# Performance work log

Hardware: AMD Instinct MI355X
Metric: run time of the kernel (lower is better)

## Reference

```python
import jax, jax.numpy as jnp
import numpy as np
import math

KERNEL_SIZES = [3, 5, 7, 7, 9, 9]
DILATIONS = [1, 2, 1, 3, 1, 2]
NUM_HEADS = 6
HEAD_DIM = 32  # in_channels 192 / 6 heads


def _neighborhood_patches(t, k, dil):
    """Equivalent of F.unfold(t, kernel_size=k, dilation=dil, padding=dil*(k//2)).
    t: [B, d, H, W] -> [B, d, k*k, H, W] (zero-padded borders, torch unfold ordering:
    patch index p = i*k + j over the kernel window, row-major)."""
    B, d, H, W = t.shape
    pad = dil * (k // 2)
    tp = jnp.pad(t, ((0, 0), (0, 0), (pad, pad), (pad, pad)))
    pats = [tp[:, :, i * dil:i * dil + H, j * dil:j * dil + W]
            for i in range(k) for j in range(k)]
    return jnp.stack(pats, axis=2)


def setup_inputs() -> dict:
    key = jax.random.key(0)
    ks = jax.random.split(key, 3 + NUM_HEADS)
    B, C, H, W = 4, 192, 96, 96
    x = jax.random.normal(ks[0], (B, C, H, W), dtype=jnp.float32)
    w_qkv = jax.random.normal(ks[1], (3 * C, C), dtype=jnp.float32) * 0.02  # 1x1 conv weight
    w_out = jax.random.normal(ks[2], (C, C), dtype=jnp.float32) * 0.02      # 1x1 conv weight
    inp = {"x": x, "w_qkv": w_qkv, "w_out": w_out}
    for i, k in enumerate(KERNEL_SIZES):
        # module inits biases to zeros; use small randn so softmax path is exercised
        inp[f"b{i}"] = jax.random.normal(ks[3 + i], (k * k,), dtype=jnp.float32) * 0.02
    return inp


def reference(x, w_qkv, w_out, b0, b1, b2, b3, b4, b5):
    biases = [b0, b1, b2, b3, b4, b5]
    B, C, H, W = x.shape
    scale = 1.0 / math.sqrt(HEAD_DIM)
    # 1x1 conv qkv projection
    qkv = jnp.einsum('bchw,oc->bohw', x, w_qkv)
    q, k, v = jnp.split(qkv, 3, axis=1)
    q = q.reshape(B, NUM_HEADS, HEAD_DIM, H, W)
    k = k.reshape(B, NUM_HEADS, HEAD_DIM, H, W)
    v = v.reshape(B, NUM_HEADS, HEAD_DIM, H, W)
    head_outs = []
    for i in range(NUM_HEADS):  # heads have structurally different (k, dilation)
        ksz, dil = KERNEL_SIZES[i], DILATIONS[i]
        kp = _neighborhood_patches(k[:, i], ksz, dil)  # [B, d, k*k, H, W]
        vp = _neighborhood_patches(v[:, i], ksz, dil)  # [B, d, k*k, H, W]
        scores = jnp.einsum('bdhw,bdphw->bphw', q[:, i], kp) * scale
        scores = scores + biases[i][None, :, None, None]
        attn = jax.nn.softmax(scores, axis=1)  # softmax over the k*k neighborhood
        head_outs.append(jnp.einsum('bphw,bdphw->bdhw', attn, vp))
    out = jnp.concatenate(head_outs, axis=1)  # [B, C, H, W]
    return jnp.einsum('bchw,oc->bohw', out, w_out)
```

## Files before the change

kernel.cpp:

```cpp
#include <hip/hip_runtime.h>
#include <hip/hip_bf16.h>
#include <math.h>

#define NPIX 9216
#define HDIM 96
#define WDIM 96
#define NHEADS 6
#define BATCH 4

typedef _Float16 f16x8 __attribute__((ext_vector_type(8)));
typedef float    f32x4 __attribute__((ext_vector_type(4)));

struct Bias6 { const float* p[6]; };

__device__ __forceinline__ void cp16(void* ldst, const void* gsrc) {
    __builtin_amdgcn_global_load_lds(
        (const __attribute__((address_space(1))) unsigned int*)gsrc,
        (__attribute__((address_space(3))) unsigned int*)ldst, 16, 0, 0);
}

__device__ __forceinline__ unsigned packf16(float a, float b) {
    _Float16 ha = (_Float16)a, hb = (_Float16)b;
    return (unsigned)*(unsigned short*)&ha | ((unsigned)*(unsigned short*)&hb << 16);
}

template<int N>
__device__ __forceinline__ void waitcnt_vm() {
    if constexpr (N == 0) asm volatile("s_waitcnt vmcnt(0)" ::: "memory");
    else if constexpr (N == 2) asm volatile("s_waitcnt vmcnt(2)" ::: "memory");
    else if constexpr (N == 3) asm volatile("s_waitcnt vmcnt(3)" ::: "memory");
    else if constexpr (N == 4) asm volatile("s_waitcnt vmcnt(4)" ::: "memory");
    else asm volatile("s_waitcnt vmcnt(0)" ::: "memory");
    __builtin_amdgcn_sched_barrier(0);
}

#define MIX_LL(acc, kk, qq) asm("v_fma_mix_f32 %0, %1, %2, %0 op_sel:[0,0,0] op_sel_hi:[1,1,0]" : "+v"(acc) : "v"(kk), "v"(qq))
#define MIX_HH(acc, kk, qq) asm("v_fma_mix_f32 %0, %1, %2, %0 op_sel:[1,1,0] op_sel_hi:[1,1,0]" : "+v"(acc) : "v"(kk), "v"(qq))
#define MIX_LF(acc, vv, ee) asm("v_fma_mix_f32 %0, %1, %2, %0 op_sel:[0,0,0] op_sel_hi:[1,0,0]" : "+v"(acc) : "v"(vv), "v"(ee))
#define MIX_HF(acc, vv, ee) asm("v_fma_mix_f32 %0, %1, %2, %0 op_sel:[1,0,0] op_sel_hi:[1,0,0]" : "+v"(acc) : "v"(vv), "v"(ee))

__global__ __launch_bounds__(256) void convert_x(
    const float* __restrict__ x, _Float16* __restrict__ Xf,
    const float* __restrict__ w1, _Float16* __restrict__ Wf1,
    const float* __restrict__ w2, _Float16* __restrict__ Wf2,
    uint4* __restrict__ guard)
{
    __shared__ float t[32][65];
    const int b  = blockIdx.z;
    const int c0 = blockIdx.y * 32;
    const int p0 = blockIdx.x * 64;
    const int tid = threadIdx.x;

    if (blockIdx.y == 0 && blockIdx.z == 0) {
        const int f = blockIdx.x * 256 + tid;
        #pragma unroll
        for (int u = 0; u < 4; ++u) {
            const int i = f * 4 + u;
            if (i < 576 * 192) Wf1[i] = (_Float16)w1[i];
            else               Wf2[i - 576 * 192] = (_Float16)w2[i - 576 * 192];
        }
        if (blockIdx.x == 0 && tid < 64)
            guard[tid] = make_uint4(0u, 0u, 0u, 0u);
    }

    const int pl = tid & 63;
    #pragma unroll
    for (int i = 0; i < 8; ++i) {
        const int c = i * 4 + (tid >> 6);
        t[c][pl] = x[((size_t)b * 192 + c0 + c) * NPIX + p0 + pl];
    }
    __syncthreads();
    const int p  = tid >> 2;
    const int cq = (tid & 3) * 8;
    f16x8 vh;
    #pragma unroll
    for (int j = 0; j < 8; ++j)
        vh[j] = (_Float16)t[cq + j][p];
    *(f16x8*)(Xf + ((size_t)b * NPIX + p0 + p) * 192 + c0 + cq) = vh;
}

template<int MODE, int M>
__global__ __launch_bounds__(256) void gemm_mfma(
    const _Float16* __restrict__ A, const _Float16* __restrict__ B,
    void* __restrict__ Yv)
{
    constexpr int MT = M / 64;
    __shared__ _Float16 sA[64 * 64];
    __shared__ _Float16 sB[128 * 64];

    const int orig = blockIdx.x;
    const int xcd = orig & 7;
    const int l = orig >> 3;
    const int m0 = (l % MT) * 64;
    const int b  = (l / MT) & 3;
    const int n0 = (xcd * 9 + l / (MT * 4)) * 128;

    const int tid  = threadIdx.x;
    const int lane = tid & 63;
    const int wid  = tid >> 6;
    const int wr = wid >> 1, wc = wid & 1;
    const int lr = lane & 15;
    const int kg = lane >> 4;

    const char* gA = (const char*)A + (size_t)m0 * 384;
    const char* gB = (const char*)B + ((size_t)b * NPIX + n0) * 384;

    f32x4 acc[2][4];
    #pragma unroll
    for (int mf = 0; mf < 2; ++mf)
        #pragma unroll
        for (int nf = 0; nf < 4; ++nf)
            acc[mf][nf] = (f32x4){0.f, 0.f, 0.f, 0.f};

    for (int ks = 0; ks < 3; ++ks) {
        if (ks) __syncthreads();
        const int kb = ks * 128;
        #pragma unroll
        for (int it = 0; it < 2; ++it) {
            const int d  = it * 256 + tid;
            const int rd = d >> 3, cd = d & 7;
            const size_t src = (size_t)rd * 384 + kb + ((cd ^ (rd & 7)) << 4);
            cp16((char*)sA + d * 16, gA + src);
        }
        #pragma unroll
        for (int it = 0; it < 4; ++it) {
            const int d  = it * 256 + tid;
            const int rd = d >> 3, cd = d & 7;
            const size_t src = (size_t)rd * 384 + kb + ((cd ^ (rd & 7)) << 4);
            cp16((char*)sB + d * 16, gB + src);
        }
        __syncthreads();
        #pragma unroll
        for (int s = 0; s < 2; ++s) {
            f16x8 aH[2], bH[4];
            #pragma unroll
            for (int mf = 0; mf < 2; ++mf) {
                const int row = wr * 32 + mf * 16 + lr;
                const int c = (s * 4 + kg) ^ (row & 7);
                aH[mf] = *(const f16x8*)((const char*)sA + row * 128 + c * 16);
            }
            #pragma unroll
            for (int nf = 0; nf < 4; ++nf) {
                const int row = wc * 64 + nf * 16 + lr;
                const int c = (s * 4 + kg) ^ (row & 7);
                bH[nf] = *(const f16x8*)((const char*)sB + row * 128 + c * 16);
            }
            #pragma unroll
            for (int mf = 0; mf < 2; ++mf)
                #pragma unroll
                for (int nf = 0; nf < 4; ++nf)
                    acc[mf][nf] = __builtin_amdgcn_mfma_f32_16x16x32_f16(aH[mf], bH[nf], acc[mf][nf], 0, 0, 0);
        }
    }

    if (MODE == 0) {
        float* Yb = (float*)Yv + ((size_t)b * M + m0 + wr * 32) * NPIX + n0 + wc * 64;
        #pragma unroll
        for (int mf = 0; mf < 2; ++mf)
            #pragma unroll
            for (int r = 0; r < 4; ++r) {
                const int row = mf * 16 + kg * 4 + r;
                #pragma unroll
                for (int nf = 0; nf < 4; ++nf)
                    Yb[(size_t)row * NPIX + nf * 16 + lr] = acc[mf][nf][r];
            }
    } else {
        #pragma unroll
        for (int mf = 0; mf < 2; ++mf) {
            const int cbase = m0 + wr * 32 + mf * 16 + kg * 4;
            unsigned* Yq = (unsigned*)Yv
                + (((size_t)b * 72 + (cbase >> 3)) * NPIX + n0 + wc * 64 + lr) * 4
                + ((kg & 1) << 1);
            #pragma unroll
            for (int nf = 0; nf < 4; ++nf) {
                Yq[(nf * 16) * 4 + 0] = packf16(acc[mf][nf][0], acc[mf][nf][1]);
                Yq[(nf * 16) * 4 + 1] = packf16(acc[mf][nf][2], acc[mf][nf][3]);
            }
        }
    }
}

#define TW 16
#define TH 16

template<int KSZ, int DIL, bool DB, int L>
__device__ __forceinline__ void attn_body(
    const uint4* __restrict__ Qq, const uint4* __restrict__ Kq,
    const uint4* __restrict__ Vq, const float* __restrict__ bias,
    const uint4* __restrict__ guard,
    _Float16* __restrict__ oh, int h0, int w0,
    uint4* __restrict__ bufs,
    unsigned (* __restrict__ out_lds)[256])
{
    constexpr int CC  = KSZ / 2;
    constexpr int HAL = CC * DIL;
    constexpr int R   = TH + 2 * HAL;
    constexpr int C   = TW + 2 * HAL;
    constexpr int RC  = R * C;
    constexpr int NN  = KSZ * KSZ;

    const int tid = threadIdx.x;
    const int tx = tid & 15;
    const int ty = tid >> 4;
    const int pix = (h0 + ty) * WDIM + (w0 + tx);
    const int lb = ty * C + tx;

    uint4 qv[4];
    #pragma unroll
    for (int p = 0; p < 4; ++p) qv[p] = Qq[(size_t)p * NPIX + pix];

    float score[NN];
    #pragma unroll
    for (int n = 0; n < NN; ++n) score[n] = bias[n] * 5.656854249492381f;

    auto STAGE = [&](int r) {
        const uint4* src = (r < 4) ? (Kq + (size_t)r * NPIX)
                                   : (Vq + (size_t)(r - 4) * NPIX);
        uint4* dst = bufs + (DB ? ((r & 1) * (L * 256)) : 0);
        #pragma unroll
        for (int it = 0; it < L; ++it) {
            const int idx = it * 256 + tid;
            const int rr = idx / C, cc = idx - rr * C;
            const int gh = h0 - HAL + rr, gw = w0 - HAL + cc;
            const bool ok = (idx < RC) && ((unsigned)gh < (unsigned)HDIM)
                                       && ((unsigned)gw < (unsigned)WDIM);
            const uint4* s = ok ? (src + gh * WDIM + gw) : guard;
            cp16(dst + idx, s);
        }
    };

    auto QK = [&](const uint4* buf, int oct) {
        const uint4 q = qv[oct];
        #pragma unroll
        for (int i = 0; i < KSZ; ++i)
            #pragma unroll
            for (int j = 0; j < KSZ; ++j) {
                const uint4 k8 = buf[lb + i * DIL * C + j * DIL];
                float s = score[i * KSZ + j];
                MIX_LL(s, k8.x, q.x); MIX_HH(s, k8.x, q.x);
                MIX_LL(s, k8.y, q.y); MIX_HH(s, k8.y, q.y);
                MIX_LL(s, k8.z, q.z); MIX_HH(s, k8.z, q.z);
                MIX_LL(s, k8.w, q.w); MIX_HH(s, k8.w, q.w);
                score[i * KSZ + j] = s;
            }
    };

    float inv = 0.f;
    auto SOFTMAX = [&]() {
        float l = 0.f;
        #pragma unroll
        for (int n = 0; n < NN; ++n) {
            const float e = exp2f(score[n] * 0.25506113952980654f);
            l += e;
            score[n] = e;
        }
        inv = 1.f / l;
    };

    auto PV = [&](const uint4* buf, int oct) {
        float a0 = 0.f, a1 = 0.f, a2 = 0.f, a3 = 0.f;
        float a4 = 0.f, a5 = 0.f, a6 = 0.f, a7 = 0.f;
        #pragma unroll
        for (int i = 0; i < KSZ; ++i)
            #pragma unroll
            for (int j = 0; j < KSZ; ++j) {
                const uint4 v8 = buf[lb + i * DIL * C + j * DIL];
                const float e = score[i * KSZ + j];
                MIX_LF(a0, v8.x, e); MIX_HF(a1, v8.x, e);
                MIX_LF(a2, v8.y, e); MIX_HF(a3, v8.y, e);
                MIX_LF(a4, v8.z, e); MIX_HF(a5, v8.z, e);
                MIX_LF(a6, v8.w, e); MIX_HF(a7, v8.w, e);
            }
        const int rr = oct & 1;
        out_lds[rr * 4 + 0][tid] = packf16(a0 * inv, a1 * inv);
        out_lds[rr * 4 + 1][tid] = packf16(a2 * inv, a3 * inv);
        out_lds[rr * 4 + 2][tid] = packf16(a4 * inv, a5 * inv);
        out_lds[rr * 4 + 3][tid] = packf16(a6 * inv, a7 * inv);
    };

    auto COOP = [&](int half) {
        #pragma unroll
        for (int it = 0; it < 2; ++it) {
            const int linear = it * 256 + tid;
            const int px = linear >> 1;
            const int c  = linear & 1;
            const int gpix = (h0 + (px >> 4)) * WDIM + w0 + (px & 15);
            uint4 val = make_uint4(out_lds[c * 4 + 0][px], out_lds[c * 4 + 1][px],
                                   out_lds[c * 4 + 2][px], out_lds[c * 4 + 3][px]);
            *((uint4*)((unsigned*)(oh + (size_t)gpix * 192)) + half * 2 + c) = val;
        }
    };

    if constexpr (DB) {
        STAGE(0);
        #pragma unroll
        for (int r = 0; r < 8; ++r) {
            if (r < 7) STAGE(r + 1);
            if (r < 7) waitcnt_vm<L>(); else waitcnt_vm<0>();
            __builtin_amdgcn_s_barrier();
            __builtin_amdgcn_sched_barrier(0);
            const uint4* buf = bufs + (r & 1) * (L * 256);
            if (r < 4) {
                QK(buf, r);
                if (r == 3) SOFTMAX();
            } else {
                PV(buf, r - 4);
                asm volatile("s_waitcnt lgkmcnt(0)" ::: "memory");
                __builtin_amdgcn_sched_barrier(0);
            }
            __builtin_amdgcn_s_barrier();
            __builtin_amdgcn_sched_barrier(0);
            if (r == 5) COOP(0);
            if (r == 7) COOP(1);
        }
    } else {
        #pragma unroll
        for (int r = 0; r < 8; ++r) {
            __syncthreads();
            if (r == 6) COOP(0);
            STAGE(r);
            __syncthreads();
            const uint4* buf = bufs;
            if (r < 4) {
                QK(buf, r);
                if (r == 3) SOFTMAX();
            } else {
                PV(buf, r - 4);
            }
        }
        __syncthreads();
        COOP(1);
    }
}

__global__ __launch_bounds__(256) void attn_kernel(
    const uint4* __restrict__ qkv, Bias6 bs, _Float16* __restrict__ ATf,
    const uint4* __restrict__ guard)
{
    __shared__ uint4 bufs[1536];
    __shared__ unsigned out_lds[8][256];

    const int orig = blockIdx.x;
    const int wg = (orig & 7) * 108 + (orig >> 3);
    const int panel = wg / 36;
    const int tile = wg - panel * 36;
    const int chunk = panel / 3, slot = panel - chunk * 3;
    int head, b;
    if (slot == 0)      { head = 4 + (chunk >> 2); b = chunk & 3; }
    else if (slot == 1) { head = 2 + (chunk >> 2); b = chunk & 3; }
    else                { head = (chunk < 4) ? 1 : 0; b = chunk & 3; }
    const int txt = tile % 6, tyt = tile / 6;
    const int w0 = txt * TW, h0 = tyt * TH;

    const uint4* base = qkv + (size_t)b * 72 * NPIX;
    const uint4* Qq = base + (size_t)(head * 4) * NPIX;
    const uint4* Kq = base + (size_t)(24 + head * 4) * NPIX;
    const uint4* Vq = base + (size_t)(48 + head * 4) * NPIX;
    _Float16* oh = ATf + (size_t)b * NPIX * 192 + head * 32;
    const float* bias = bs.p[head];

    switch (head) {
        case 0: attn_body<3, 1, true, 2>(Qq, Kq, Vq, bias, guard, oh, h0, w0, bufs, out_lds); break;
        case 1: attn_body<5, 2, true, 3>(Qq, Kq, Vq, bias, guard, oh, h0, w0, bufs, out_lds); break;
        case 2: attn_body<7, 1, true, 2>(Qq, Kq, Vq, bias, guard, oh, h0, w0, bufs, out_lds); break;
        case 3: attn_body<7, 3, false, 5>(Qq, Kq, Vq, bias, guard, oh, h0, w0, bufs, out_lds); break;
        case 4: attn_body<9, 1, true, 3>(Qq, Kq, Vq, bias, guard, oh, h0, w0, bufs, out_lds); break;
        case 5: attn_body<9, 2, false, 4>(Qq, Kq, Vq, bias, guard, oh, h0, w0, bufs, out_lds); break;
    }
}

extern "C" void kernel_launch(void* const* d_in, const int* in_sizes, int n_in,
                              void* d_out, int out_size, void* d_ws, size_t ws_size,
                              hipStream_t stream) {
    const float* x     = (const float*)d_in[0];
    const float* w_qkv = (const float*)d_in[1];
    const float* w_out = (const float*)d_in[2];
    Bias6 bs;
    for (int i = 0; i < 6; ++i) bs.p[i] = (const float*)d_in[3 + i];
    float* out = (float*)d_out;

    char* ws = (char*)d_ws;
    uint4*    QKV = (uint4*)ws;         ws += (size_t)BATCH * 72 * NPIX * 16;
    _Float16* Xf  = (_Float16*)ws;      ws += (size_t)BATCH * NPIX * 192 * 2;
    _Float16* ATf = (_Float16*)ws;      ws += (size_t)BATCH * NPIX * 192 * 2;
    _Float16* Wf1 = (_Float16*)ws;      ws += (size_t)576 * 192 * 2;
    _Float16* Wf2 = (_Float16*)ws;      ws += (size_t)192 * 192 * 2;
    uint4* guard  = (uint4*)ws;         ws += 1024;

    convert_x<<<dim3(NPIX / 64, 192 / 32, BATCH), 256, 0, stream>>>(
        x, Xf, w_qkv, Wf1, w_out, Wf2, guard);

    gemm_mfma<1, 576><<<dim3(8 * (576 / 64) * 4 * 9), 256, 0, stream>>>(
        Wf1, Xf, (void*)QKV);

    attn_kernel<<<dim3(864), 256, 0, stream>>>(QKV, bs, ATf, guard);

    gemm_mfma<0, 192><<<dim3(8 * (192 / 64) * 4 * 9), 256, 0, stream>>>(
        Wf2, ATf, (void*)out);
}
```

Measured before the change: 83.27 us.

## Fuse fp32-to-fp16 conversion of inputs and weights into GEMM tile loads

Removes the separate convert_x kernel and its fp16 workspace copies of x and the weights. The GEMMs now read fp32 directly, convert to fp16 in registers and write swizzled tiles to LDS, and the guard reset moves into the first GEMM. This saves one launch and a full write and read of the converted activation tensor. In exchange, the async global-to-LDS copies for those operands become synchronous register loads, and with MT=9 each x tile is re-read and re-converted by nine M-tile blocks.

```diff
diff --git a/kernel.cpp b/kernel.cpp
--- a/kernel.cpp
+++ b/kernel.cpp
@@ -39,50 +39,10 @@
 #define MIX_LF(acc, vv, ee) asm("v_fma_mix_f32 %0, %1, %2, %0 op_sel:[0,0,0] op_sel_hi:[1,0,0]" : "+v"(acc) : "v"(vv), "v"(ee))
 #define MIX_HF(acc, vv, ee) asm("v_fma_mix_f32 %0, %1, %2, %0 op_sel:[1,0,0] op_sel_hi:[1,0,0]" : "+v"(acc) : "v"(vv), "v"(ee))
 
-__global__ __launch_bounds__(256) void convert_x(
-    const float* __restrict__ x, _Float16* __restrict__ Xf,
-    const float* __restrict__ w1, _Float16* __restrict__ Wf1,
-    const float* __restrict__ w2, _Float16* __restrict__ Wf2,
-    uint4* __restrict__ guard)
-{
-    __shared__ float t[32][65];
-    const int b  = blockIdx.z;
-    const int c0 = blockIdx.y * 32;
-    const int p0 = blockIdx.x * 64;
-    const int tid = threadIdx.x;
-
-    if (blockIdx.y == 0 && blockIdx.z == 0) {
-        const int f = blockIdx.x * 256 + tid;
-        #pragma unroll
-        for (int u = 0; u < 4; ++u) {
-            const int i = f * 4 + u;
-            if (i < 576 * 192) Wf1[i] = (_Float16)w1[i];
-            else               Wf2[i - 576 * 192] = (_Float16)w2[i - 576 * 192];
-        }
-        if (blockIdx.x == 0 && tid < 64)
-            guard[tid] = make_uint4(0u, 0u, 0u, 0u);
-    }
-
-    const int pl = tid & 63;
-    #pragma unroll
-    for (int i = 0; i < 8; ++i) {
-        const int c = i * 4 + (tid >> 6);
-        t[c][pl] = x[((size_t)b * 192 + c0 + c) * NPIX + p0 + pl];
-    }
-    __syncthreads();
-    const int p  = tid >> 2;
-    const int cq = (tid & 3) * 8;
-    f16x8 vh;
-    #pragma unroll
-    for (int j = 0; j < 8; ++j)
-        vh[j] = (_Float16)t[cq + j][p];
-    *(f16x8*)(Xf + ((size_t)b * NPIX + p0 + p) * 192 + c0 + cq) = vh;
-}
-
-template<int MODE, int M>
+template<int MODE, int M, bool BF32>
 __global__ __launch_bounds__(256) void gemm_mfma(
-    const _Float16* __restrict__ A, const _Float16* __restrict__ B,
-    void* __restrict__ Yv)
+    const float* __restrict__ A32, const void* __restrict__ Bp,
+    void* __restrict__ Yv, uint4* __restrict__ guard)
 {
     constexpr int MT = M / 64;
     __shared__ _Float16 sA[64 * 64];
@@ -102,8 +62,8 @@
     const int lr = lane & 15;
     const int kg = lane >> 4;
 
-    const char* gA = (const char*)A + (size_t)m0 * 384;
-    const char* gB = (const char*)B + ((size_t)b * NPIX + n0) * 384;
+    if (MODE == 1 && orig == 0 && tid < 64)
+        guard[tid] = make_uint4(0u, 0u, 0u, 0u);
 
     f32x4 acc[2][4];
     #pragma unroll
@@ -112,22 +72,60 @@
         for (int nf = 0; nf < 4; ++nf)
             acc[mf][nf] = (f32x4){0.f, 0.f, 0.f, 0.f};
 
+    const int ar = tid >> 2;
+    const int ac = (tid & 3) * 16;
+    const int bpx = tid & 127;
+    const int bc0 = (tid >> 7) * 32;
+
     for (int ks = 0; ks < 3; ++ks) {
         if (ks) __syncthreads();
-        const int kb = ks * 128;
-        #pragma unroll
-        for (int it = 0; it < 2; ++it) {
-            const int d  = it * 256 + tid;
-            const int rd = d >> 3, cd = d & 7;
-            const size_t src = (size_t)rd * 384 + kb + ((cd ^ (rd & 7)) << 4);
-            cp16((char*)sA + d * 16, gA + src);
-        }
-        #pragma unroll
-        for (int it = 0; it < 4; ++it) {
-            const int d  = it * 256 + tid;
-            const int rd = d >> 3, cd = d & 7;
-            const size_t src = (size_t)rd * 384 + kb + ((cd ^ (rd & 7)) << 4);
-            cp16((char*)sB + d * 16, gB + src);
+        {
+            const float* g = A32 + (size_t)(m0 + ar) * 192 + ks * 64 + ac;
+            float v[16];
+            #pragma unroll
+            for (int j = 0; j < 4; ++j) {
+                f32x4 t = *(const f32x4*)(g + j * 4);
+                v[j * 4 + 0] = t[0]; v[j * 4 + 1] = t[1];
+                v[j * 4 + 2] = t[2]; v[j * 4 + 3] = t[3];
+            }
+            #pragma unroll
+            for (int q = 0; q < 2; ++q) {
+                const int cd = (tid & 3) * 2 + q;
+                uint4 u = make_uint4(
+                    packf16(v[q * 8 + 0], v[q * 8 + 1]),
+                    packf16(v[q * 8 + 2], v[q * 8 + 3]),
+                    packf16(v[q * 8 + 4], v[q * 8 + 5]),
+                    packf16(v[q * 8 + 6], v[q * 8 + 7]));
+                *(uint4*)((char*)sA + ar * 128 + ((cd ^ (ar & 7)) << 4)) = u;
+            }
+        }
+        if constexpr (BF32) {
+            const float* g = (const float*)Bp
+                + ((size_t)b * 192 + ks * 64 + bc0) * NPIX + n0 + bpx;
+            float v[32];
+            #pragma unroll
+            for (int c = 0; c < 32; ++c)
+                v[c] = g[(size_t)c * NPIX];
+            #pragma unroll
+            for (int q = 0; q < 4; ++q) {
+                const int cd = (bc0 >> 3) + q;
+                uint4 u = make_uint4(
+                    packf16(v[q * 8 + 0], v[q * 8 + 1]),
+                    packf16(v[q * 8 + 2], v[q * 8 + 3]),
+                    packf16(v[q * 8 + 4], v[q * 8 + 5]),
+                    packf16(v[q * 8 + 6], v[q * 8 + 7]));
+                *(uint4*)((char*)sB + bpx * 128 + ((cd ^ (bpx & 7)) << 4)) = u;
+            }
+        } else {
+            const char* gB = (const char*)Bp + ((size_t)b * NPIX + n0) * 384;
+            const int kb = ks * 128;
+            #pragma unroll
+            for (int it = 0; it < 4; ++it) {
+                const int d  = it * 256 + tid;
+                const int rd = d >> 3, cd = d & 7;
+                const size_t src = (size_t)rd * 384 + kb + ((cd ^ (rd & 7)) << 4);
+                cp16((char*)sB + d * 16, gB + src);
+            }
         }
         __syncthreads();
         #pragma unroll
@@ -381,20 +379,14 @@
 
     char* ws = (char*)d_ws;
     uint4*    QKV = (uint4*)ws;         ws += (size_t)BATCH * 72 * NPIX * 16;
-    _Float16* Xf  = (_Float16*)ws;      ws += (size_t)BATCH * NPIX * 192 * 2;
     _Float16* ATf = (_Float16*)ws;      ws += (size_t)BATCH * NPIX * 192 * 2;
-    _Float16* Wf1 = (_Float16*)ws;      ws += (size_t)576 * 192 * 2;
-    _Float16* Wf2 = (_Float16*)ws;      ws += (size_t)192 * 192 * 2;
     uint4* guard  = (uint4*)ws;         ws += 1024;
 
-    convert_x<<<dim3(NPIX / 64, 192 / 32, BATCH), 256, 0, stream>>>(
-        x, Xf, w_qkv, Wf1, w_out, Wf2, guard);
-
-    gemm_mfma<1, 576><<<dim3(8 * (576 / 64) * 4 * 9), 256, 0, stream>>>(
-        Wf1, Xf, (void*)QKV);
+    gemm_mfma<1, 576, true><<<dim3(8 * (576 / 64) * 4 * 9), 256, 0, stream>>>(
+        w_qkv, (const void*)x, (void*)QKV, guard);
 
     attn_kernel<<<dim3(864), 256, 0, stream>>>(QKV, bs, ATf, guard);
 
-    gemm_mfma<0, 192><<<dim3(8 * (192 / 64) * 4 * 9), 256, 0, stream>>>(
-        Wf2, ATf, (void*)out);
-}
+    gemm_mfma<0, 192, false><<<dim3(8 * (192 / 64) * 4 * 9), 256, 0, stream>>>(
+        w_out, (const void*)ATf, (void*)out, guard);
+}
```

Measured after the change: 84.12 us. About the same (+1.0%).
